# Performance work log

Hardware: AMD Instinct MI355X
Metric: run time of the kernel (lower is better)

Reference implementation:

```python
import jax, jax.numpy as jnp
import numpy as np


def setup_inputs() -> dict:
    key = jax.random.key(0)
    k1, k2, k3 = jax.random.split(key, 3)
    B, C, H, W = 64, 512, 28, 28
    K = 32
    std = 1.0 / (K * C) ** 0.5
    x = jax.random.normal(k1, (B, C, H, W), dtype=jnp.float32)
    codewords = jax.random.uniform(k2, (K, C), dtype=jnp.float32, minval=-std, maxval=std)
    scale = jax.random.uniform(k3, (K,), dtype=jnp.float32, minval=-1.0, maxval=0.0)
    return {"x": x, "codewords": codewords, "scale": scale}


def reference(x, codewords, scale):
    # x: (B, C, H, W) -> descriptors (B, N, C)
    B, C, H, W = x.shape
    K = codewords.shape[0]
    xd = x.reshape(B, C, H * W).transpose(0, 2, 1)  # (B, N, C)

    # scaled L2: scale_k * ||x_n - c_k||^2, expanded without (B,N,K,C) intermediate
    x_sq = jnp.sum(xd * xd, axis=-1, keepdims=True)            # (B, N, 1)
    c_sq = jnp.sum(codewords * codewords, axis=-1)             # (K,)
    xc = jnp.einsum("bnc,kc->bnk", xd, codewords)              # (B, N, K)
    dist = scale * (x_sq - 2.0 * xc + c_sq)                    # (B, N, K)

    A = jax.nn.softmax(dist, axis=2)                           # (B, N, K)

    # encoded_k = sum_n A[b,n,k] * (x[b,n] - c[k])
    wx = jnp.einsum("bnk,bnc->bkc", A, xd)                     # (B, K, C)
    wsum = jnp.sum(A, axis=1)                                  # (B, K)
    encoded = wx - wsum[:, :, None] * codewords[None, :, :]    # (B, K, C)
    return encoded
```

## Files before the change

kernel.cpp:

```cpp
#include <hip/hip_runtime.h>

#define BB 64
#define CC 512
#define NPIX 784
#define KK 32
#define NSA 13
#define AS 800
#define NSTEP 24
#define RS 66
#define XT_BUF (64*RS)

typedef __attribute__((ext_vector_type(8))) short short8;
typedef __attribute__((ext_vector_type(4))) float floatx4;

#define WSUM_OFF (BB * KK * AS)

__device__ __forceinline__ unsigned short f2bf(float f) {
    union { float f; unsigned u; } v; v.f = f;
    return (unsigned short)((v.u + 0x7FFFu + ((v.u >> 16) & 1u)) >> 16);
}
__device__ __forceinline__ short8 pack8(const float4& a, const float4& b) {
    short8 r;
    r[0] = (short)f2bf(a.x); r[1] = (short)f2bf(a.y);
    r[2] = (short)f2bf(a.z); r[3] = (short)f2bf(a.w);
    r[4] = (short)f2bf(b.x); r[5] = (short)f2bf(b.y);
    r[6] = (short)f2bf(b.z); r[7] = (short)f2bf(b.w);
    return r;
}

__global__ __launch_bounds__(256, 4) void kA(const float* __restrict__ x,
                                             const float* __restrict__ cw,
                                             const float* __restrict__ scale,
                                             unsigned short* __restrict__ Ag)
{
    __shared__ __align__(16) float xt[2 * XT_BUF];
    __shared__ float csq_p[8][KK];
    __shared__ float csq_l[KK];
    __shared__ float wredA[4][KK];

    const int t    = threadIdx.x;
    const int lane = t & 63, w = t >> 6;
    const int col  = lane & 15, quad = lane >> 4;
    const int split = blockIdx.x, b = blockIdx.y;
    const int p0    = (split < 12) ? split * 64 : 720;

    if (split == 0 && t < 64) {
        const short8 z = {0, 0, 0, 0, 0, 0, 0, 0};
        const int k = t >> 1, off = (t & 1) * 8;
        *(short8*)&Ag[(size_t)b * KK * AS + (size_t)k * AS + NPIX + off] = z;
    }

    const float* xb = x + (size_t)b * CC * NPIX + p0;
    const int r0 = t >> 4, p4 = t & 15;

#pragma unroll
    for (int j = 0; j < 4; ++j) {
        const int row = r0 + j * 16;
        const float4 v = *(const float4*)&xb[(size_t)row * NPIX + p4 * 4];
        float* d = &xt[row * RS + p4 * 4];
        *(float2*)&d[0] = make_float2(v.x, v.y);
        *(float2*)&d[2] = make_float2(v.z, v.w);
    }
    {
        const int k = t & 31, part = t >> 5;
        const float* cp = cw + k * CC + part * 64;
        float s = 0.f;
#pragma unroll
        for (int i = 0; i < 16; ++i) {
            const float4 v = *(const float4*)&cp[i * 4];
            s += v.x * v.x + v.y * v.y + v.z * v.z + v.w * v.w;
        }
        csq_p[part][k] = s;
    }
    __syncthreads();
    if (t < KK) {
        float s = 0.f;
#pragma unroll
        for (int p = 0; p < 8; ++p) s += csq_p[p][t];
        csq_l[t] = s;
    }

    floatx4 acc0 = {0.f, 0.f, 0.f, 0.f};
    floatx4 acc1 = {0.f, 0.f, 0.f, 0.f};
    float xsqp = 0.f;
    const int wcol = w * 16 + col;

#pragma unroll
    for (int ch = 0; ch < 8; ++ch) {
        const int cur = ch & 1;
        float4 pre[4];
        if (ch < 7) {
            const float* xs = xb + (size_t)(ch + 1) * 64 * NPIX;
#pragma unroll
            for (int j = 0; j < 4; ++j)
                pre[j] = *(const float4*)&xs[(size_t)(r0 + j * 16) * NPIX + p4 * 4];
        }
#pragma unroll
        for (int kl = 0; kl < 2; ++kl) {
            const int kcg = ch * 2 + kl;
            float va[8];
            const float* src = &xt[cur * XT_BUF + (kl * 32 + quad * 8) * RS + wcol];
#pragma unroll
            for (int j = 0; j < 8; ++j) va[j] = src[j * RS];
            short8 a;
#pragma unroll
            for (int j = 0; j < 8; ++j) { xsqp += va[j] * va[j]; a[j] = (short)f2bf(va[j]); }
            const int cb = kcg * 32 + quad * 8;
            const short8 b0 = pack8(*(const float4*)&cw[col * CC + cb],
                                    *(const float4*)&cw[col * CC + cb + 4]);
            const short8 b1 = pack8(*(const float4*)&cw[(col + 16) * CC + cb],
                                    *(const float4*)&cw[(col + 16) * CC + cb + 4]);
            acc0 = __builtin_amdgcn_mfma_f32_16x16x32_bf16(a, b0, acc0, 0, 0, 0);
            acc1 = __builtin_amdgcn_mfma_f32_16x16x32_bf16(a, b1, acc1, 0, 0, 0);
        }
        if (ch < 7) {
            const int nb = cur ^ 1;
#pragma unroll
            for (int j = 0; j < 4; ++j) {
                float* d = &xt[nb * XT_BUF + (r0 + j * 16) * RS + p4 * 4];
                *(float2*)&d[0] = make_float2(pre[j].x, pre[j].y);
                *(float2*)&d[2] = make_float2(pre[j].z, pre[j].w);
            }
            __syncthreads();
        }
    }

    xsqp += __shfl_xor(xsqp, 16);
    xsqp += __shfl_xor(xsqp, 32);

    const float s0 = scale[col], s1 = scale[col + 16];
    const float q0 = csq_l[col], q1 = csq_l[col + 16];

    unsigned short* Ab = Ag + (size_t)b * KK * AS + p0 + w * 16;
    float ts0 = 0.f, ts1 = 0.f;
#pragma unroll
    for (int r = 0; r < 4; ++r) {
        const float xq = __shfl(xsqp, quad * 4 + r);
        const float d0 = s0 * (xq + q0 - 2.f * acc0[r]);
        const float d1 = s1 * (xq + q1 - 2.f * acc1[r]);
        float mx = fmaxf(d0, d1);
        mx = fmaxf(mx, __shfl_xor(mx, 1));
        mx = fmaxf(mx, __shfl_xor(mx, 2));
        mx = fmaxf(mx, __shfl_xor(mx, 4));
        mx = fmaxf(mx, __shfl_xor(mx, 8));
        const float e0 = __expf(d0 - mx), e1 = __expf(d1 - mx);
        float sm = e0 + e1;
        sm += __shfl_xor(sm, 1);
        sm += __shfl_xor(sm, 2);
        sm += __shfl_xor(sm, 4);
        sm += __shfl_xor(sm, 8);
        const float inv = 1.f / sm;
        const float a0 = e0 * inv, a1 = e1 * inv;
        Ab[col * AS + quad * 4 + r]        = f2bf(a0);
        Ab[(col + 16) * AS + quad * 4 + r] = f2bf(a1);
        ts0 += a0; ts1 += a1;
    }

    ts0 += __shfl_xor(ts0, 16); ts0 += __shfl_xor(ts0, 32);
    ts1 += __shfl_xor(ts1, 16); ts1 += __shfl_xor(ts1, 32);
    if (quad == 0) { wredA[w][col] = ts0; wredA[w][col + 16] = ts1; }
    __syncthreads();
    if (t < KK) {
        float s;
        if (split < 12) s = wredA[0][t] + wredA[1][t] + wredA[2][t] + wredA[3][t];
        else            s = wredA[3][t];
        float* wsf = (float*)(Ag + WSUM_OFF);
        wsf[(size_t)(split * BB + b) * KK + t] = s;
    }
}

__global__ __launch_bounds__(256) void kB(const float* __restrict__ x,
                                          const float* __restrict__ cw,
                                          const unsigned short* __restrict__ Ag,
                                          float* __restrict__ out)
{
    __shared__ float wsum_l[KK];

    const int t    = threadIdx.x;
    const int lane = t & 63, w = t >> 6;
    const int col  = lane & 15, quad = lane >> 4;
    const int cch  = blockIdx.x, b = blockIdx.y;

    const unsigned short* Ab = Ag + (size_t)b * KK * AS;

    if (t < KK) {
        const float* wsf = (const float*)(Ag + WSUM_OFF);
        float s = 0.f;
#pragma unroll
        for (int sp = 0; sp < NSA; ++sp) s += wsf[(size_t)(sp * BB + b) * KK + t];
        wsum_l[t] = s;
    }

    const int c = cch * 64 + w * 16 + col;
    const float* xp = x + ((size_t)b * CC + c) * NPIX;
    const unsigned short* a0p = Ab + (size_t)col * AS;
    const unsigned short* a1p = Ab + (size_t)(col + 16) * AS;
    const int qo = quad * 8;

    floatx4 acc0 = {0.f, 0.f, 0.f, 0.f};
    floatx4 acc1 = {0.f, 0.f, 0.f, 0.f};
#pragma unroll 6
    for (int s = 0; s < NSTEP; ++s) {
        const int off = s * 32 + qo;
        const short8 av0 = *(const short8*)&a0p[off];
        const short8 av1 = *(const short8*)&a1p[off];
        const float4 xv0 = *(const float4*)&xp[off];
        const float4 xv1 = *(const float4*)&xp[off + 4];
        const short8 bv = pack8(xv0, xv1);
        acc0 = __builtin_amdgcn_mfma_f32_16x16x32_bf16(av0, bv, acc0, 0, 0, 0);
        acc1 = __builtin_amdgcn_mfma_f32_16x16x32_bf16(av1, bv, acc1, 0, 0, 0);
    }
    {
        const int off = NSTEP * 32 + qo;
        const short8 av0 = *(const short8*)&a0p[off];
        const short8 av1 = *(const short8*)&a1p[off];
        float4 xv0 = make_float4(0.f, 0.f, 0.f, 0.f);
        float4 xv1 = make_float4(0.f, 0.f, 0.f, 0.f);
        if (quad < 2) {
            xv0 = *(const float4*)&xp[off];
            xv1 = *(const float4*)&xp[off + 4];
        }
        const short8 bv = pack8(xv0, xv1);
        acc0 = __builtin_amdgcn_mfma_f32_16x16x32_bf16(av0, bv, acc0, 0, 0, 0);
        acc1 = __builtin_amdgcn_mfma_f32_16x16x32_bf16(av1, bv, acc1, 0, 0, 0);
    }

    __syncthreads();

    float* ob = out + (size_t)b * KK * CC + c;
    const float* cp = cw + c;
#pragma unroll
    for (int r = 0; r < 4; ++r) {
        const int k0 = quad * 4 + r;
        ob[(size_t)k0 * CC]        = acc0[r] - wsum_l[k0]      * cp[(size_t)k0 * CC];
        ob[(size_t)(k0 + 16) * CC] = acc1[r] - wsum_l[k0 + 16] * cp[(size_t)(k0 + 16) * CC];
    }
}

extern "C" void kernel_launch(void* const* d_in, const int* in_sizes, int n_in,
                              void* d_out, int out_size, void* d_ws, size_t ws_size,
                              hipStream_t stream) {
    const float* x     = (const float*)d_in[0];
    const float* cw    = (const float*)d_in[1];
    const float* scale = (const float*)d_in[2];
    float* out = (float*)d_out;
    unsigned short* Ag = (unsigned short*)d_ws;

    kA<<<dim3(NSA, BB), dim3(256), 0, stream>>>(x, cw, scale, Ag);
    kB<<<dim3(8, BB), dim3(256), 0, stream>>>(x, cw, Ag, out);
}
```

Before: 193.9 us.

## Deepen global-load prefetch to three chunks and commit before compute

The kA kernel now issues global loads for x three channel-chunks ahead, rotating through three register sets. Each chunk is written into the idle LDS buffer before the MFMA compute on the current buffer, instead of after it. The __syncthreads is replaced by an explicit lgkmcnt wait plus s_barrier, so the barrier does not also wait on outstanding global loads. The goal is to hide more global memory latency, at the cost of about 48 extra VGPRs that may hurt occupancy under the 256x4 launch bound.

```diff
diff --git a/kernel.cpp b/kernel.cpp
--- a/kernel.cpp
+++ b/kernel.cpp
@@ -6,9 +6,8 @@
 #define KK 32
 #define NSA 13
 #define AS 800
+#define RS 66
 #define NSTEP 24
-#define RS 66
-#define XT_BUF (64*RS)
 
 typedef __attribute__((ext_vector_type(8))) short short8;
 typedef __attribute__((ext_vector_type(4))) float floatx4;
@@ -28,12 +27,27 @@
     return r;
 }
 
+#define ISSUE(chk, P0, P1, P2, P3) {                                           \
+    const float* _s = xb + (size_t)(chk) * 64 * NPIX + p4 * 4;                 \
+    P0 = *(const float4*)&_s[(size_t)(r0     ) * NPIX];                        \
+    P1 = *(const float4*)&_s[(size_t)(r0 + 16) * NPIX];                        \
+    P2 = *(const float4*)&_s[(size_t)(r0 + 32) * NPIX];                        \
+    P3 = *(const float4*)&_s[(size_t)(r0 + 48) * NPIX]; }
+
+#define COMMIT1(bf, RR, P) {                                                   \
+    float* _d = &xt[bf][(RR) * RS + p4 * 4];                                   \
+    *(float2*)&_d[0] = make_float2(P.x, P.y);                                  \
+    *(float2*)&_d[2] = make_float2(P.z, P.w); }
+#define COMMIT(bf, P0, P1, P2, P3) {                                           \
+    COMMIT1(bf, r0,      P0); COMMIT1(bf, r0 + 16, P1);                        \
+    COMMIT1(bf, r0 + 32, P2); COMMIT1(bf, r0 + 48, P3); }
+
 __global__ __launch_bounds__(256, 4) void kA(const float* __restrict__ x,
                                              const float* __restrict__ cw,
                                              const float* __restrict__ scale,
                                              unsigned short* __restrict__ Ag)
 {
-    __shared__ __align__(16) float xt[2 * XT_BUF];
+    __shared__ __align__(16) float xt[2][64 * RS];
     __shared__ float csq_p[8][KK];
     __shared__ float csq_l[KK];
     __shared__ float wredA[4][KK];
@@ -50,17 +64,6 @@
         *(short8*)&Ag[(size_t)b * KK * AS + (size_t)k * AS + NPIX + off] = z;
     }
 
-    const float* xb = x + (size_t)b * CC * NPIX + p0;
-    const int r0 = t >> 4, p4 = t & 15;
-
-#pragma unroll
-    for (int j = 0; j < 4; ++j) {
-        const int row = r0 + j * 16;
-        const float4 v = *(const float4*)&xb[(size_t)row * NPIX + p4 * 4];
-        float* d = &xt[row * RS + p4 * 4];
-        *(float2*)&d[0] = make_float2(v.x, v.y);
-        *(float2*)&d[2] = make_float2(v.z, v.w);
-    }
     {
         const int k = t & 31, part = t >> 5;
         const float* cp = cw + k * CC + part * 64;
@@ -80,32 +83,47 @@
         csq_l[t] = s;
     }
 
+    const float* xb = x + (size_t)b * CC * NPIX + p0;
+    const int r0 = t >> 4, p4 = t & 15;
+    const int wcol = w * 16 + col;
+
+    float4 pA0, pA1, pA2, pA3, pB0, pB1, pB2, pB3, pC0, pC1, pC2, pC3;
+    ISSUE(0, pA0, pA1, pA2, pA3);
+    ISSUE(1, pB0, pB1, pB2, pB3);
+    ISSUE(2, pC0, pC1, pC2, pC3);
+    COMMIT(0, pA0, pA1, pA2, pA3);
+    asm volatile("s_waitcnt lgkmcnt(0)" ::: "memory");
+    __builtin_amdgcn_s_barrier();
+    asm volatile("" ::: "memory");
+
     floatx4 acc0 = {0.f, 0.f, 0.f, 0.f};
     floatx4 acc1 = {0.f, 0.f, 0.f, 0.f};
     float xsqp = 0.f;
-    const int wcol = w * 16 + col;
 
 #pragma unroll
     for (int ch = 0; ch < 8; ++ch) {
-        const int cur = ch & 1;
-        float4 pre[4];
-        if (ch < 7) {
-            const float* xs = xb + (size_t)(ch + 1) * 64 * NPIX;
-#pragma unroll
-            for (int j = 0; j < 4; ++j)
-                pre[j] = *(const float4*)&xs[(size_t)(r0 + j * 16) * NPIX + p4 * 4];
+        if (ch + 3 < 8) {
+            if (ch % 3 == 0)      { ISSUE(ch + 3, pA0, pA1, pA2, pA3); }
+            else if (ch % 3 == 1) { ISSUE(ch + 3, pB0, pB1, pB2, pB3); }
+            else                  { ISSUE(ch + 3, pC0, pC1, pC2, pC3); }
+        }
+        if (ch + 1 < 8) {
+            const int nb = (ch + 1) & 1;
+            if ((ch + 1) % 3 == 0)      { COMMIT(nb, pA0, pA1, pA2, pA3); }
+            else if ((ch + 1) % 3 == 1) { COMMIT(nb, pB0, pB1, pB2, pB3); }
+            else                        { COMMIT(nb, pC0, pC1, pC2, pC3); }
         }
 #pragma unroll
         for (int kl = 0; kl < 2; ++kl) {
-            const int kcg = ch * 2 + kl;
+            const int kc = ch * 2 + kl;
+            const float* srcl = &xt[ch & 1][(kl * 32 + quad * 8) * RS + wcol];
             float va[8];
-            const float* src = &xt[cur * XT_BUF + (kl * 32 + quad * 8) * RS + wcol];
-#pragma unroll
-            for (int j = 0; j < 8; ++j) va[j] = src[j * RS];
+#pragma unroll
+            for (int j = 0; j < 8; ++j) va[j] = srcl[j * RS];
             short8 a;
 #pragma unroll
             for (int j = 0; j < 8; ++j) { xsqp += va[j] * va[j]; a[j] = (short)f2bf(va[j]); }
-            const int cb = kcg * 32 + quad * 8;
+            const int cb = kc * 32 + quad * 8;
             const short8 b0 = pack8(*(const float4*)&cw[col * CC + cb],
                                     *(const float4*)&cw[col * CC + cb + 4]);
             const short8 b1 = pack8(*(const float4*)&cw[(col + 16) * CC + cb],
@@ -113,16 +131,9 @@
             acc0 = __builtin_amdgcn_mfma_f32_16x16x32_bf16(a, b0, acc0, 0, 0, 0);
             acc1 = __builtin_amdgcn_mfma_f32_16x16x32_bf16(a, b1, acc1, 0, 0, 0);
         }
-        if (ch < 7) {
-            const int nb = cur ^ 1;
-#pragma unroll
-            for (int j = 0; j < 4; ++j) {
-                float* d = &xt[nb * XT_BUF + (r0 + j * 16) * RS + p4 * 4];
-                *(float2*)&d[0] = make_float2(pre[j].x, pre[j].y);
-                *(float2*)&d[2] = make_float2(pre[j].z, pre[j].w);
-            }
-            __syncthreads();
-        }
+        asm volatile("s_waitcnt lgkmcnt(0)" ::: "memory");
+        __builtin_amdgcn_s_barrier();
+        asm volatile("" ::: "memory");
     }
 
     xsqp += __shfl_xor(xsqp, 16);
```

Result: no change. 196.6 us (+1.4%).
